# Kernel tuning notes

Measured on AMD Instinct MI355X. Metric: run time of the kernel, lower is better.

The kernel has to match this reference:

```python
import jax, jax.numpy as jnp
import numpy as np

# Model dims (match init_kwargs)
INPUT_CAPS = 2048
INPUT_DIM = 16
OUTPUT_CAPS = 16
OUTPUT_DIM = 16
D = OUTPUT_CAPS * OUTPUT_DIM  # 256
BATCH = 64


def setup_inputs() -> dict:
    key = jax.random.key(0)
    k1, k2 = jax.random.split(key)
    caps_output = jax.random.normal(k1, (BATCH, INPUT_CAPS, INPUT_DIM), dtype=jnp.float32)
    stdv = 1.0 / np.sqrt(INPUT_CAPS)
    weights = jax.random.uniform(k2, (INPUT_CAPS, INPUT_DIM, D),
                                 minval=-stdv, maxval=stdv, dtype=jnp.float32)
    return {"caps_output": caps_output, "weights": weights}


def reference(caps_output, weights):
    # u_predict[b,c,:] = caps_output[b,c,:] @ weights[c]  -> [B, IC, D]
    u = jnp.einsum('bci,cio->bco', caps_output, weights)
    # Gram matrix C = A^T A  -> [B, D, D], symmetric PSD (real eigenvalues)
    C = jnp.einsum('bcd,bce->bde', u, u)
    # Top eigenpair. Original code uses np.linalg.eig per batch on CPU and
    # selects the largest eigenvalue; C is symmetric so eigh is the faithful
    # (and efficient) form. eigh returns ascending order -> take last column.
    e_vals, e_vecs = jnp.linalg.eigh(C)
    v = e_vecs[:, :, -1]  # [B, D] dominant eigenvector
    # Fix eigenvector sign deterministically (largest-|component| positive)
    idx = jnp.argmax(jnp.abs(v), axis=1)
    sgn = jnp.sign(jnp.take_along_axis(v, idx[:, None], axis=1))
    v = v * sgn
    return v.reshape(BATCH, OUTPUT_CAPS, OUTPUT_DIM)
```

## Files before the change

kernel.cpp:

```cpp
#include <hip/hip_runtime.h>

#define NB  64
#define IC  2048
#define ID  16
#define DD  256
#define DDSQ 65536
#define PB  (DDSQ * NB)
#define NSQ 11
#define NPI 7

typedef __attribute__((ext_vector_type(8))) short          s16x8;
typedef __attribute__((ext_vector_type(4))) float          f32x4;
typedef __attribute__((ext_vector_type(4))) unsigned short us4;
typedef __attribute__((ext_vector_type(8))) unsigned short us8;

__device__ __forceinline__ unsigned short f2b(float f) {
    union { float f; unsigned u; } c; c.f = f;
    const unsigned u = c.u + 0x7FFFu + ((c.u >> 16) & 1u);
    return (unsigned short)(u >> 16);
}
__device__ __forceinline__ float b2f(unsigned short h) {
    union { unsigned u; float f; } c; c.u = ((unsigned)h) << 16;
    return c.f;
}
__device__ __forceinline__ unsigned f2pk(float f) {
    const unsigned short h = f2b(f);
    const unsigned short l = f2b(f - b2f(h));
    return ((unsigned)h << 16) | (unsigned)l;
}

__global__ __launch_bounds__(256, 4) void u_kernel(const float* __restrict__ caps,
                                                   const float* __restrict__ W,
                                                   unsigned* __restrict__ U) {
    const int c = blockIdx.x;
    const int t = threadIdx.x;
    __shared__ float xsT[ID][64];
    {
        const int b = t >> 2, q = (t & 3) * 4;
        const float4 x4 = *(const float4*)&caps[((size_t)b * IC + c) * ID + q];
        xsT[q + 0][b] = x4.x; xsT[q + 1][b] = x4.y;
        xsT[q + 2][b] = x4.z; xsT[q + 3][b] = x4.w;
    }
    __syncthreads();
    float a[64];
#pragma unroll
    for (int b = 0; b < 64; ++b) a[b] = 0.f;
#pragma unroll
    for (int i = 0; i < ID; ++i) {
        const float wi = W[((size_t)c * ID + i) * DD + t];
#pragma unroll
        for (int g = 0; g < 16; ++g) {
            const float4 x = *(const float4*)&xsT[i][g * 4];
            a[g * 4 + 0] = fmaf(x.x, wi, a[g * 4 + 0]);
            a[g * 4 + 1] = fmaf(x.y, wi, a[g * 4 + 1]);
            a[g * 4 + 2] = fmaf(x.z, wi, a[g * 4 + 2]);
            a[g * 4 + 3] = fmaf(x.w, wi, a[g * 4 + 3]);
        }
    }
#pragma unroll
    for (int b = 0; b < 64; ++b)
        U[((size_t)b * IC + c) * DD + t] = f2pk(a[b]);
}

__global__ __launch_bounds__(256, 4)
void cm64_kernel(const unsigned* __restrict__ Up,
                 unsigned short* __restrict__ Ch, unsigned short* __restrict__ Cl,
                 float* __restrict__ Sc) {
    const int id   = blockIdx.x;
    const int bb   = id & 63;
    const int tile = id >> 6;
    int tr, tc;
    if (tile < 4)      { tr = 0; tc = tile; }
    else if (tile < 7) { tr = 1; tc = tile - 3; }
    else if (tile < 9) { tr = 2; tc = tile - 5; }
    else               { tr = 3; tc = 3; }
    const int d0 = tr * 64, e0 = tc * 64;
    const int t    = threadIdx.x;
    const int lane = t & 63, wid = t >> 6;
    const int wm = wid >> 1, wn = wid & 1;
    const int fr = lane & 15, kg = lane >> 4;
    const int sl8 = lane & 7, qg = lane >> 3;
    const size_t mb = (size_t)bb * DDSQ;

    __shared__ unsigned short Ah[64][40];
    __shared__ unsigned short Al[64][40];
    __shared__ unsigned short Bh[64][40];
    __shared__ unsigned short Bl[64][40];
    __shared__ float red[256];

    const f32x4 z4 = {0.f, 0.f, 0.f, 0.f};
    f32x4 acc[2][2];
#pragma unroll
    for (int m = 0; m < 2; ++m)
#pragma unroll
        for (int n = 0; n < 2; ++n) acc[m][n] = z4;

    const unsigned* Ub = Up + (size_t)bb * IC * DD;
    unsigned va[2][4], vb[2][4];
    auto loadU = [&](int kb) {
#pragma unroll
        for (int s = 0; s < 2; ++s) {
            const int row = wid * 8 + sl8 + 32 * s;
#pragma unroll
            for (int j = 0; j < 4; ++j)
                va[s][j] = Ub[(size_t)(kb + 4 * qg + j) * DD + d0 + row];
        }
#pragma unroll
        for (int s = 0; s < 2; ++s) {
            const int row = wid * 8 + sl8 + 32 * s;
#pragma unroll
            for (int j = 0; j < 4; ++j)
                vb[s][j] = Ub[(size_t)(kb + 4 * qg + j) * DD + e0 + row];
        }
    };

    loadU(0);
    for (int kb = 0; kb < IC; kb += 32) {
        __syncthreads();
#pragma unroll
        for (int s = 0; s < 2; ++s) {
            const int row = wid * 8 + sl8 + 32 * s;
            us4 h, l;
#pragma unroll
            for (int j = 0; j < 4; ++j) {
                h[j] = (unsigned short)(va[s][j] >> 16);
                l[j] = (unsigned short)(va[s][j] & 0xFFFFu);
            }
            *(us4*)&Ah[row][4 * qg] = h;
            *(us4*)&Al[row][4 * qg] = l;
        }
#pragma unroll
        for (int s = 0; s < 2; ++s) {
            const int row = wid * 8 + sl8 + 32 * s;
            us4 h, l;
#pragma unroll
            for (int j = 0; j < 4; ++j) {
                h[j] = (unsigned short)(vb[s][j] >> 16);
                l[j] = (unsigned short)(vb[s][j] & 0xFFFFu);
            }
            *(us4*)&Bh[row][4 * qg] = h;
            *(us4*)&Bl[row][4 * qg] = l;
        }
        __syncthreads();
        if (kb + 32 < IC) loadU(kb + 32);
        s16x8 ah[2], al[2], bh[2], bl[2];
#pragma unroll
        for (int m = 0; m < 2; ++m) {
            const int r = wm * 32 + m * 16 + fr;
            ah[m] = *(const s16x8*)&Ah[r][kg * 8];
            al[m] = *(const s16x8*)&Al[r][kg * 8];
        }
#pragma unroll
        for (int n = 0; n < 2; ++n) {
            const int r = wn * 32 + n * 16 + fr;
            bh[n] = *(const s16x8*)&Bh[r][kg * 8];
            bl[n] = *(const s16x8*)&Bl[r][kg * 8];
        }
#pragma unroll
        for (int m = 0; m < 2; ++m)
#pragma unroll
            for (int n = 0; n < 2; ++n) {
                acc[m][n] = __builtin_amdgcn_mfma_f32_16x16x32_bf16(ah[m], bh[n], acc[m][n], 0, 0, 0);
                acc[m][n] = __builtin_amdgcn_mfma_f32_16x16x32_bf16(ah[m], bl[n], acc[m][n], 0, 0, 0);
                acc[m][n] = __builtin_amdgcn_mfma_f32_16x16x32_bf16(al[m], bh[n], acc[m][n], 0, 0, 0);
            }
    }

    float ts = 0.f;
    const int row_l = wm * 32 + (lane >> 4) * 4;
    const int col_l = wn * 32 + fr;
    const bool mir = (tr != tc);
#pragma unroll
    for (int m = 0; m < 2; ++m)
#pragma unroll
        for (int n = 0; n < 2; ++n) {
            const int gr0 = d0 + row_l + m * 16;
            const int gc  = e0 + col_l + n * 16;
            us4 h4, l4;
#pragma unroll
            for (int r = 0; r < 4; ++r) {
                const float e = acc[m][n][r];
                const unsigned short h = f2b(e);
                const unsigned short l = f2b(e - b2f(h));
                const size_t o = mb + (size_t)(gr0 + r) * DD + gc;
                Ch[o] = h; Cl[o] = l;
                h4[r] = h; l4[r] = l;
                if (gr0 + r == gc) ts += e;
            }
            if (mir) {
                const size_t o2 = mb + (size_t)gc * DD + gr0;
                *(us4*)&Ch[o2] = h4;
                *(us4*)&Cl[o2] = l4;
            }
        }
    if (tr == tc) {
        red[t] = ts;
        __syncthreads();
        for (int s2 = 128; s2 > 0; s2 >>= 1) {
            if (t < s2) red[t] += red[t + s2];
            __syncthreads();
        }
        if (t == 0) atomicAdd(&Sc[bb], red[0]);
    }
}

__global__ __launch_bounds__(256, 4)
void sqm_kernel(const unsigned short* __restrict__ Dh, const unsigned short* __restrict__ Dl,
                unsigned short* __restrict__ Eh, unsigned short* __restrict__ El,
                const float* __restrict__ s_in, float* __restrict__ s_out) {
    const int id   = blockIdx.x;
    const int bb   = id & 63;
    const int tile = id >> 6;
    int tr, tc;
    if (tile < 4)      { tr = 0; tc = tile; }
    else if (tile < 7) { tr = 1; tc = tile - 3; }
    else if (tile < 9) { tr = 2; tc = tile - 5; }
    else               { tr = 3; tc = 3; }
    const int d0 = tr * 64, e0 = tc * 64;
    const int t    = threadIdx.x;
    const int lane = t & 63, wid = t >> 6;
    const int wm = wid >> 1, wn = wid & 1;
    const int fr = lane & 15, kg = lane >> 4;
    const size_t mb = (size_t)bb * DDSQ;

    __shared__ unsigned short Ah[64][72];
    __shared__ unsigned short Al[64][72];
    __shared__ unsigned short Bh[64][72];
    __shared__ unsigned short Bl[64][72];
    __shared__ float red[256];

    const f32x4 z4 = {0.f, 0.f, 0.f, 0.f};
    f32x4 acc[2][2];
#pragma unroll
    for (int m = 0; m < 2; ++m)
#pragma unroll
        for (int n = 0; n < 2; ++n) acc[m][n] = z4;

    const float s   = s_in[bb];
    const float inv = 1.f / (s * s);
    const int row = t >> 2, q = t & 3;

    for (int kb = 0; kb < DD; kb += 64) {
        const size_t ga = mb + (size_t)(d0 + row) * DD + kb + q * 8;
        const size_t gb = mb + (size_t)(e0 + row) * DD + kb + q * 8;
        const int4 rah0 = *(const int4*)&Dh[ga];
        const int4 rah1 = *(const int4*)&Dh[ga + 32];
        const int4 ral0 = *(const int4*)&Dl[ga];
        const int4 ral1 = *(const int4*)&Dl[ga + 32];
        const int4 rbh0 = *(const int4*)&Dh[gb];
        const int4 rbh1 = *(const int4*)&Dh[gb + 32];
        const int4 rbl0 = *(const int4*)&Dl[gb];
        const int4 rbl1 = *(const int4*)&Dl[gb + 32];
        __syncthreads();
        *(int4*)&Ah[row][q * 8]      = rah0;
        *(int4*)&Ah[row][q * 8 + 32] = rah1;
        *(int4*)&Al[row][q * 8]      = ral0;
        *(int4*)&Al[row][q * 8 + 32] = ral1;
        *(int4*)&Bh[row][q * 8]      = rbh0;
        *(int4*)&Bh[row][q * 8 + 32] = rbh1;
        *(int4*)&Bl[row][q * 8]      = rbl0;
        *(int4*)&Bl[row][q * 8 + 32] = rbl1;
        __syncthreads();

#pragma unroll
        for (int h = 0; h < 2; ++h) {
            const int ko = kg * 8 + 32 * h;
            s16x8 ah[2], al[2], bh[2], bl[2];
#pragma unroll
            for (int m = 0; m < 2; ++m) {
                const int r = wm * 32 + m * 16 + fr;
                ah[m] = *(const s16x8*)&Ah[r][ko];
                al[m] = *(const s16x8*)&Al[r][ko];
            }
#pragma unroll
            for (int n = 0; n < 2; ++n) {
                const int r = wn * 32 + n * 16 + fr;
                bh[n] = *(const s16x8*)&Bh[r][ko];
                bl[n] = *(const s16x8*)&Bl[r][ko];
            }
#pragma unroll
            for (int m = 0; m < 2; ++m)
#pragma unroll
                for (int n = 0; n < 2; ++n) {
                    acc[m][n] = __builtin_amdgcn_mfma_f32_16x16x32_bf16(ah[m], bh[n], acc[m][n], 0, 0, 0);
                    acc[m][n] = __builtin_amdgcn_mfma_f32_16x16x32_bf16(ah[m], bl[n], acc[m][n], 0, 0, 0);
                    acc[m][n] = __builtin_amdgcn_mfma_f32_16x16x32_bf16(al[m], bh[n], acc[m][n], 0, 0, 0);
                }
        }
    }

    float ts = 0.f;
    const int row_l = wm * 32 + (lane >> 4) * 4;
    const int col_l = wn * 32 + fr;
    const bool mir = (tr != tc);
#pragma unroll
    for (int m = 0; m < 2; ++m)
#pragma unroll
        for (int n = 0; n < 2; ++n) {
            const int gr0 = d0 + row_l + m * 16;
            const int gc  = e0 + col_l + n * 16;
            us4 h4, l4;
#pragma unroll
            for (int r = 0; r < 4; ++r) {
                const float e = acc[m][n][r] * inv;
                const unsigned short h = f2b(e);
                const unsigned short l = f2b(e - b2f(h));
                const size_t o = mb + (size_t)(gr0 + r) * DD + gc;
                Eh[o] = h; El[o] = l;
                h4[r] = h; l4[r] = l;
                if (gr0 + r == gc) ts += e;
            }
            if (mir) {
                const size_t o2 = mb + (size_t)gc * DD + gr0;
                *(us4*)&Eh[o2] = h4;
                *(us4*)&El[o2] = l4;
            }
        }
    if (tr == tc) {
        red[t] = ts;
        __syncthreads();
        for (int s2 = 128; s2 > 0; s2 >>= 1) {
            if (t < s2) red[t] += red[t + s2];
            __syncthreads();
        }
        if (t == 0) atomicAdd(&s_out[bb], red[0]);
    }
}

__global__ __launch_bounds__(1024, 1)
void finish_kernel(const unsigned short* __restrict__ Dh,
                   const unsigned short* __restrict__ Dl,
                   float* __restrict__ out) {
    const int b = blockIdx.x, t = threadIdx.x;
    const int row = t >> 2, q = t & 3;
    const size_t mb = (size_t)b * DDSQ;
    __shared__ float vs[DD];
    __shared__ float red[DD];
    __shared__ int   ridx[DD];
    if (t < DD) {
        red[t] = b2f(Dh[mb + (size_t)t * DD + t]) + b2f(Dl[mb + (size_t)t * DD + t]);
        ridx[t] = t;
    }
    __syncthreads();
    for (int s = 128; s > 0; s >>= 1) {
        if (t < s && red[t + s] > red[t]) { red[t] = red[t + s]; ridx[t] = ridx[t + s]; }
        __syncthreads();
    }
    const int jmax0 = ridx[0];
    __syncthreads();
    if (t < DD)
        vs[t] = b2f(Dh[mb + (size_t)jmax0 * DD + t]) + b2f(Dl[mb + (size_t)jmax0 * DD + t]);
    __syncthreads();

    const unsigned short* rh = Dh + mb + (size_t)row * DD + q * 64;
    const unsigned short* rl = Dl + mb + (size_t)row * DD + q * 64;
    for (int it = 0; it < NPI; ++it) {
        float a = 0.f;
        const float* vq = vs + q * 64;
#pragma unroll
        for (int j = 0; j < 64; j += 8) {
            const us8 h8 = *(const us8*)&rh[j];
            const us8 l8 = *(const us8*)&rl[j];
            a = fmaf(b2f(h8[0]) + b2f(l8[0]), vq[j + 0], a);
            a = fmaf(b2f(h8[1]) + b2f(l8[1]), vq[j + 1], a);
            a = fmaf(b2f(h8[2]) + b2f(l8[2]), vq[j + 2], a);
            a = fmaf(b2f(h8[3]) + b2f(l8[3]), vq[j + 3], a);
            a = fmaf(b2f(h8[4]) + b2f(l8[4]), vq[j + 4], a);
            a = fmaf(b2f(h8[5]) + b2f(l8[5]), vq[j + 5], a);
            a = fmaf(b2f(h8[6]) + b2f(l8[6]), vq[j + 6], a);
            a = fmaf(b2f(h8[7]) + b2f(l8[7]), vq[j + 7], a);
        }
        a += __shfl_xor(a, 1);
        a += __shfl_xor(a, 2);
        __syncthreads();
        if (q == 0) vs[row] = a;
        __syncthreads();
    }

    if (t < DD) red[t] = vs[t] * vs[t];
    __syncthreads();
    for (int s = 128; s > 0; s >>= 1) {
        if (t < s) red[t] += red[t + s];
        __syncthreads();
    }
    const float nrm = sqrtf(red[0]);
    __syncthreads();
    if (t < DD) { red[t] = fabsf(vs[t]); ridx[t] = t; }
    __syncthreads();
    for (int s = 128; s > 0; s >>= 1) {
        if (t < s && red[t + s] > red[t]) { red[t] = red[t + s]; ridx[t] = ridx[t + s]; }
        __syncthreads();
    }
    const float sgn = (vs[ridx[0]] < 0.f) ? -1.f : 1.f;
    if (t < DD) out[(size_t)b * DD + t] = sgn * vs[t] / nrm;
}

extern "C" void kernel_launch(void* const* d_in, const int* in_sizes, int n_in,
                              void* d_out, int out_size, void* d_ws, size_t ws_size,
                              hipStream_t stream) {
    const float* caps = (const float*)d_in[0];
    const float* W    = (const float*)d_in[1];
    float* out = (float*)d_out;
    float* ws  = (float*)d_ws;

    unsigned* Up = (unsigned*)ws;
    unsigned short* Xh = (unsigned short*)(ws + (size_t)8 * PB);
    unsigned short* Xl = Xh + (size_t)NB * DDSQ;
    unsigned short* Yh = (unsigned short*)(ws + (size_t)9 * PB);
    unsigned short* Yl = Yh + (size_t)NB * DDSQ;
    float* Sc = ws + (size_t)10 * PB;

    hipMemsetAsync(Sc, 0, 2048 * sizeof(float), stream);

    u_kernel<<<IC, 256, 0, stream>>>(caps, W, Up);
    cm64_kernel<<<640, 256, 0, stream>>>(Up, Xh, Xl, Sc);

    unsigned short* ph = Xh; unsigned short* pl = Xl;
    unsigned short* qh = Yh; unsigned short* ql = Yl;
    for (int it = 0; it < NSQ; ++it) {
        sqm_kernel<<<640, 256, 0, stream>>>(ph, pl, qh, ql,
                                            Sc + it * 64, Sc + (it + 1) * 64);
        unsigned short* t1 = ph; ph = qh; qh = t1;
        unsigned short* t2 = pl; pl = ql; ql = t2;
    }

    finish_kernel<<<NB, 1024, 0, stream>>>(ph, pl, out);
}
```

Measured before the change: 324.7 us.

## Split Gram matrix K-reduction across two blocks and fuse first squaring

The Gram-matrix kernel now splits the 2048-long reduction into two halves, launching twice as many blocks and accumulating into an fp32 buffer with atomics. A new first-squaring kernel reads that fp32 matrix, converts it to hi/lo bf16 on the fly and performs the first squaring step, replacing the first sqm launch. The aim is better occupancy for the Gram step, which had only 640 blocks doing long serial K loops. The cost is an extra memset of a 16M-float buffer, many scalar global atomics, and fp32 reads in the first squaring step.

```diff
diff --git a/kernel.cpp b/kernel.cpp
--- a/kernel.cpp
+++ b/kernel.cpp
@@ -27,6 +27,12 @@
     const unsigned short h = f2b(f);
     const unsigned short l = f2b(f - b2f(h));
     return ((unsigned)h << 16) | (unsigned)l;
+}
+__device__ __forceinline__ void tri_map(int tile, int& tr, int& tc) {
+    if (tile < 4)      { tr = 0; tc = tile; }
+    else if (tile < 7) { tr = 1; tc = tile - 3; }
+    else if (tile < 9) { tr = 2; tc = tile - 5; }
+    else               { tr = 3; tc = 3; }
 }
 
 __global__ __launch_bounds__(256, 4) void u_kernel(const float* __restrict__ caps,
@@ -63,17 +69,13 @@
 }
 
 __global__ __launch_bounds__(256, 4)
-void cm64_kernel(const unsigned* __restrict__ Up,
-                 unsigned short* __restrict__ Ch, unsigned short* __restrict__ Cl,
-                 float* __restrict__ Sc) {
+void cm64sk_kernel(const unsigned* __restrict__ Up,
+                   float* __restrict__ F, float* __restrict__ Sc) {
     const int id   = blockIdx.x;
     const int bb   = id & 63;
-    const int tile = id >> 6;
-    int tr, tc;
-    if (tile < 4)      { tr = 0; tc = tile; }
-    else if (tile < 7) { tr = 1; tc = tile - 3; }
-    else if (tile < 9) { tr = 2; tc = tile - 5; }
-    else               { tr = 3; tc = 3; }
+    const int tk   = id >> 6;
+    const int tile = tk >> 1, kch = tk & 1;
+    int tr, tc; tri_map(tile, tr, tc);
     const int d0 = tr * 64, e0 = tc * 64;
     const int t    = threadIdx.x;
     const int lane = t & 63, wid = t >> 6;
@@ -96,6 +98,7 @@
         for (int n = 0; n < 2; ++n) acc[m][n] = z4;
 
     const unsigned* Ub = Up + (size_t)bb * IC * DD;
+    const int k0 = kch * (IC / 2);
     unsigned va[2][4], vb[2][4];
     auto loadU = [&](int kb) {
 #pragma unroll
@@ -114,8 +117,8 @@
         }
     };
 
-    loadU(0);
-    for (int kb = 0; kb < IC; kb += 32) {
+    loadU(k0);
+    for (int kb = k0; kb < k0 + IC / 2; kb += 32) {
         __syncthreads();
 #pragma unroll
         for (int s = 0; s < 2; ++s) {
@@ -142,7 +145,7 @@
             *(us4*)&Bl[row][4 * qg] = l;
         }
         __syncthreads();
-        if (kb + 32 < IC) loadU(kb + 32);
+        if (kb + 32 < k0 + IC / 2) loadU(kb + 32);
         s16x8 ah[2], al[2], bh[2], bl[2];
 #pragma unroll
         for (int m = 0; m < 2; ++m) {
@@ -166,6 +169,7 @@
             }
     }
 
+    float* Fb = F + mb;
     float ts = 0.f;
     const int row_l = wm * 32 + (lane >> 4) * 4;
     const int col_l = wn * 32 + fr;
@@ -176,21 +180,134 @@
         for (int n = 0; n < 2; ++n) {
             const int gr0 = d0 + row_l + m * 16;
             const int gc  = e0 + col_l + n * 16;
-            us4 h4, l4;
 #pragma unroll
             for (int r = 0; r < 4; ++r) {
                 const float e = acc[m][n][r];
+                atomicAdd(&Fb[(size_t)(gr0 + r) * DD + gc], e);
+                if (mir) atomicAdd(&Fb[(size_t)gc * DD + gr0 + r], e);
+                if (gr0 + r == gc) ts += e;
+            }
+        }
+    if (tr == tc) {
+        red[t] = ts;
+        __syncthreads();
+        for (int s2 = 128; s2 > 0; s2 >>= 1) {
+            if (t < s2) red[t] += red[t + s2];
+            __syncthreads();
+        }
+        if (t == 0) atomicAdd(&Sc[bb], red[0]);
+    }
+}
+
+__global__ __launch_bounds__(256, 4)
+void sqf_kernel(const float* __restrict__ F,
+                unsigned short* __restrict__ Eh, unsigned short* __restrict__ El,
+                const float* __restrict__ s_in, float* __restrict__ s_out) {
+    const int id   = blockIdx.x;
+    const int bb   = id & 63;
+    const int tile = id >> 6;
+    int tr, tc; tri_map(tile, tr, tc);
+    const int d0 = tr * 64, e0 = tc * 64;
+    const int t    = threadIdx.x;
+    const int lane = t & 63, wid = t >> 6;
+    const int wm = wid >> 1, wn = wid & 1;
+    const int fr = lane & 15, kg = lane >> 4;
+    const size_t mb = (size_t)bb * DDSQ;
+
+    __shared__ unsigned short Ah[64][40];
+    __shared__ unsigned short Al[64][40];
+    __shared__ unsigned short Bh[64][40];
+    __shared__ unsigned short Bl[64][40];
+    __shared__ float red[256];
+
+    const f32x4 z4 = {0.f, 0.f, 0.f, 0.f};
+    f32x4 acc[2][2];
+#pragma unroll
+    for (int m = 0; m < 2; ++m)
+#pragma unroll
+        for (int n = 0; n < 2; ++n) acc[m][n] = z4;
+
+    const float s   = s_in[bb];
+    const float inv = 1.f / (s * s);
+
+    for (int kb = 0; kb < DD; kb += 32) {
+        float4 va[2], vb[2];
+#pragma unroll
+        for (int i = 0; i < 2; ++i) {
+            const int slot = t + i * 256;
+            const int row = slot >> 3, q8 = slot & 7;
+            va[i] = *(const float4*)&F[mb + (size_t)(d0 + row) * DD + kb + q8 * 4];
+            vb[i] = *(const float4*)&F[mb + (size_t)(e0 + row) * DD + kb + q8 * 4];
+        }
+        __syncthreads();
+#pragma unroll
+        for (int i = 0; i < 2; ++i) {
+            const int slot = t + i * 256;
+            const int row = slot >> 3, q8 = slot & 7;
+            us4 h, l;
+            h.x = f2b(va[i].x); l.x = f2b(va[i].x - b2f(h.x));
+            h.y = f2b(va[i].y); l.y = f2b(va[i].y - b2f(h.y));
+            h.z = f2b(va[i].z); l.z = f2b(va[i].z - b2f(h.z));
+            h.w = f2b(va[i].w); l.w = f2b(va[i].w - b2f(h.w));
+            *(us4*)&Ah[row][q8 * 4] = h;
+            *(us4*)&Al[row][q8 * 4] = l;
+            h.x = f2b(vb[i].x); l.x = f2b(vb[i].x - b2f(h.x));
+            h.y = f2b(vb[i].y); l.y = f2b(vb[i].y - b2f(h.y));
+            h.z = f2b(vb[i].z); l.z = f2b(vb[i].z - b2f(h.z));
+            h.w = f2b(vb[i].w); l.w = f2b(vb[i].w - b2f(h.w));
+            *(us4*)&Bh[row][q8 * 4] = h;
+            *(us4*)&Bl[row][q8 * 4] = l;
+        }
+        __syncthreads();
+
+        s16x8 ah[2], al[2], bh[2], bl[2];
+#pragma unroll
+        for (int m = 0; m < 2; ++m) {
+            const int r = wm * 32 + m * 16 + fr;
+            ah[m] = *(const s16x8*)&Ah[r][kg * 8];
+            al[m] = *(const s16x8*)&Al[r][kg * 8];
+        }
+#pragma unroll
+        for (int n = 0; n < 2; ++n) {
+            const int r = wn * 32 + n * 16 + fr;
+            bh[n] = *(const s16x8*)&Bh[r][kg * 8];
+            bl[n] = *(const s16x8*)&Bl[r][kg * 8];
+        }
+#pragma unroll
+        for (int m = 0; m < 2; ++m)
+#pragma unroll
+            for (int n = 0; n < 2; ++n) {
+                acc[m][n] = __builtin_amdgcn_mfma_f32_16x16x32_bf16(ah[m], bh[n], acc[m][n], 0, 0, 0);
+                acc[m][n] = __builtin_amdgcn_mfma_f32_16x16x32_bf16(ah[m], bl[n], acc[m][n], 0, 0, 0);
+                acc[m][n] = __builtin_amdgcn_mfma_f32_16x16x32_bf16(al[m], bh[n], acc[m][n], 0, 0, 0);
+            }
+    }
+
+    float ts = 0.f;
+    const int row_l = wm * 32 + (lane >> 4) * 4;
+    const int col_l = wn * 32 + fr;
+    const bool mir = (tr != tc);
+#pragma unroll
+    for (int m = 0; m < 2; ++m)
+#pragma unroll
+        for (int n = 0; n < 2; ++n) {
+            const int gr0 = d0 + row_l + m * 16;
+            const int gc  = e0 + col_l + n * 16;
+            us4 h4, l4;
+#pragma unroll
+            for (int r = 0; r < 4; ++r) {
+                const float e = acc[m][n][r] * inv;
                 const unsigned short h = f2b(e);
                 const unsigned short l = f2b(e - b2f(h));
                 const size_t o = mb + (size_t)(gr0 + r) * DD + gc;
-                Ch[o] = h; Cl[o] = l;
+                Eh[o] = h; El[o] = l;
                 h4[r] = h; l4[r] = l;
                 if (gr0 + r == gc) ts += e;
             }
             if (mir) {
                 const size_t o2 = mb + (size_t)gc * DD + gr0;
-                *(us4*)&Ch[o2] = h4;
-                *(us4*)&Cl[o2] = l4;
+                *(us4*)&Eh[o2] = h4;
+                *(us4*)&El[o2] = l4;
             }
         }
     if (tr == tc) {
@@ -200,7 +317,7 @@
             if (t < s2) red[t] += red[t + s2];
             __syncthreads();
         }
-        if (t == 0) atomicAdd(&Sc[bb], red[0]);
+        if (t == 0) atomicAdd(&s_out[bb], red[0]);
     }
 }
 
@@ -211,11 +328,7 @@
     const int id   = blockIdx.x;
     const int bb   = id & 63;
     const int tile = id >> 6;
-    int tr, tc;
-    if (tile < 4)      { tr = 0; tc = tile; }
-    else if (tile < 7) { tr = 1; tc = tile - 3; }
-    else if (tile < 9) { tr = 2; tc = tile - 5; }
-    else               { tr = 3; tc = 3; }
+    int tr, tc; tri_map(tile, tr, tc);
     const int d0 = tr * 64, e0 = tc * 64;
     const int t    = threadIdx.x;
     const int lane = t & 63, wid = t >> 6;
@@ -404,20 +517,24 @@
     float* ws  = (float*)d_ws;
 
     unsigned* Up = (unsigned*)ws;
-    unsigned short* Xh = (unsigned short*)(ws + (size_t)8 * PB);
-    unsigned short* Xl = Xh + (size_t)NB * DDSQ;
-    unsigned short* Yh = (unsigned short*)(ws + (size_t)9 * PB);
-    unsigned short* Yl = Yh + (size_t)NB * DDSQ;
+    float* F = ws + (size_t)8 * PB;
+    unsigned short* B0h = (unsigned short*)(ws + (size_t)9 * PB);
+    unsigned short* B0l = B0h + (size_t)NB * DDSQ;
+    unsigned short* B1h = (unsigned short*)(ws + (size_t)8 * PB);
+    unsigned short* B1l = B1h + (size_t)NB * DDSQ;
     float* Sc = ws + (size_t)10 * PB;
 
     hipMemsetAsync(Sc, 0, 2048 * sizeof(float), stream);
+    hipMemsetAsync(F, 0, (size_t)PB * sizeof(float), stream);
 
     u_kernel<<<IC, 256, 0, stream>>>(caps, W, Up);
-    cm64_kernel<<<640, 256, 0, stream>>>(Up, Xh, Xl, Sc);
-
-    unsigned short* ph = Xh; unsigned short* pl = Xl;
-    unsigned short* qh = Yh; unsigned short* ql = Yl;
-    for (int it = 0; it < NSQ; ++it) {
+    cm64sk_kernel<<<1280, 256, 0, stream>>>(Up, F, Sc);
+
+    sqf_kernel<<<640, 256, 0, stream>>>(F, B0h, B0l, Sc, Sc + 64);
+
+    unsigned short* ph = B0h; unsigned short* pl = B0l;
+    unsigned short* qh = B1h; unsigned short* ql = B1l;
+    for (int it = 1; it < NSQ; ++it) {
         sqm_kernel<<<640, 256, 0, stream>>>(ph, pl, qh, ql,
                                             Sc + it * 64, Sc + (it + 1) * 64);
         unsigned short* t1 = ph; ph = qh; qh = t1;
```

After: 365.8 us. 1.13x slower.
